# Performance work log

Measured on AMD Instinct MI355X. Metric: run time of the kernel, lower is better.

Reference implementation:

```python
import jax, jax.numpy as jnp
import numpy as np

BS, S, D, H = 2, 2048, 1024, 16
DH = D // H  # 64


def setup_inputs() -> dict:
    key = jax.random.key(0)
    k1, k2, k3 = jax.random.split(key, 3)
    x = jax.random.normal(k1, (BS, S, D), dtype=jnp.float32)
    w_qkv = jax.random.normal(k2, (D, H, 3 * DH), dtype=jnp.float32) * (D ** -0.5)
    b_qkv = jnp.zeros((H, 3 * DH), dtype=jnp.float32)
    w_out = jax.random.normal(k3, (H, DH, D), dtype=jnp.float32) * (D ** -0.5)
    b_out = jnp.zeros((D,), dtype=jnp.float32)
    return {"x": x, "w_qkv": w_qkv, "b_qkv": b_qkv, "w_out": w_out, "b_out": b_out}


def reference(x, w_qkv, b_qkv, w_out, b_out):
    dtype = x.dtype
    # QKV projection: DenseGeneral(features=(H, 3*DH)) -> [B, S, H, 3*DH]
    qkv = jnp.einsum("bsd,dhf->bshf", x, w_qkv) + b_qkv
    q, k, v = jnp.split(qkv, 3, axis=-1)  # each [B, S, H, DH]

    scale = DH ** -0.5
    q = (q * scale).astype(jnp.float32)
    k = k.astype(jnp.float32)
    # Full causal attention with fp32 scores (as in original)
    weights = jnp.einsum("bqhd,bkhd->bhqk", q, k)  # [B, H, S, S]
    causal = jnp.tril(jnp.ones((S, S), dtype=bool))[None, None, :, :]
    weights = jnp.where(causal, weights, jnp.finfo(jnp.float32).min)
    weights = jax.nn.softmax(weights, axis=-1).astype(dtype)
    attn = jnp.einsum("bhqk,bkhd->bqhd", weights, v).astype(dtype)

    # Output projection: DenseGeneral(D, axis=(-2, -1))
    out = jnp.einsum("bqhd,hdo->bqo", attn, w_out) + b_out
    return out
```

## Files before the change

kernel.cpp:

```cpp
#include <hip/hip_runtime.h>
#include <hip/hip_bf16.h>
#include <stdint.h>

#define NBS 2
#define SEQ 2048
#define DMODEL 1024
#define NH 16
#define DHEAD 64
#define MROWS (NBS*SEQ)
#define NQKV (NH*3*DHEAD)

typedef __bf16 bf16;
typedef __bf16 bf16x8 __attribute__((ext_vector_type(8)));
typedef float f32x4 __attribute__((ext_vector_type(4)));
typedef float f32x16 __attribute__((ext_vector_type(16)));
typedef unsigned int u32x2 __attribute__((ext_vector_type(2)));

#define LOG2E 1.44269504088896f
#define QSCALE (0.125f * LOG2E)

static __device__ __forceinline__ void gload_lds16(const bf16* g, bf16* l) {
    __builtin_amdgcn_global_load_lds(
        (const __attribute__((address_space(1))) uint32_t*)g,
        (__attribute__((address_space(3))) uint32_t*)l, 16, 0, 0);
}

static __device__ __forceinline__ bf16x8 ld_b8(const bf16* p) {
    return __builtin_bit_cast(bf16x8, *(const uint4*)p);
}

static __device__ __forceinline__ uint32_t pk_bf16(float lo, float hi) {
    unsigned short l = __builtin_bit_cast(unsigned short, (bf16)lo);
    unsigned short h = __builtin_bit_cast(unsigned short, (bf16)hi);
    return ((uint32_t)h << 16) | (uint32_t)l;
}

static __device__ __forceinline__ u32x2 lane_swap32(uint32_t a, uint32_t b, int lane) {
#if __has_builtin(__builtin_amdgcn_permlane32_swap)
    return __builtin_amdgcn_permlane32_swap(a, b, false, false);
#else
    uint32_t sa = __shfl_xor(a, 32), sb = __shfl_xor(b, 32);
    u32x2 r;
    r.x = (lane >= 32) ? sb : a;
    r.y = (lane >= 32) ? b : sa;
    return r;
#endif
}


__global__ void k_cvt(const float* __restrict__ in, bf16* __restrict__ out, int n4) {
    int i = blockIdx.x * blockDim.x + threadIdx.x;
    if (i < n4) {
        float4 v = ((const float4*)in)[i];
        ushort4 o;
        o.x = __builtin_bit_cast(unsigned short, (bf16)v.x);
        o.y = __builtin_bit_cast(unsigned short, (bf16)v.y);
        o.z = __builtin_bit_cast(unsigned short, (bf16)v.z);
        o.w = __builtin_bit_cast(unsigned short, (bf16)v.w);
        ((ushort4*)out)[i] = o;
    }
}

__global__ void k_tcvt(const float* __restrict__ in, bf16* __restrict__ out, int R, int C) {
    __shared__ float t[32][33];
    int tx = threadIdx.x, ty = threadIdx.y;
    int r0 = blockIdx.y * 32, c0 = blockIdx.x * 32;
#pragma unroll
    for (int i = 0; i < 4; i++)
        t[ty + i*8][tx] = in[(size_t)(r0 + ty + i*8) * C + (c0 + tx)];
    __syncthreads();
#pragma unroll
    for (int i = 0; i < 4; i++)
        out[(size_t)(c0 + ty + i*8) * R + (r0 + tx)] = (bf16)t[tx][ty + i*8];
}

__global__ void k_tcvt_qkv(const float* __restrict__ in, bf16* __restrict__ out) {
    __shared__ float t[32][33];
    int tx = threadIdx.x, ty = threadIdx.y;
    int r0 = blockIdx.y * 32, c0 = blockIdx.x * 32;
#pragma unroll
    for (int i = 0; i < 4; i++)
        t[ty + i*8][tx] = in[(size_t)(r0 + ty + i*8) * NQKV + (c0 + tx)];
    __syncthreads();
#pragma unroll
    for (int i = 0; i < 4; i++) {
        int c = c0 + ty + i*8;
        int h = c / 192, f = c % 192;
        int cperm = ((f >> 6) << 10) + (h << 6) + (f & 63);
        out[(size_t)cperm * DMODEL + (r0 + tx)] = (bf16)t[tx][ty + i*8];
    }
}

template<int KD>
static __device__ __forceinline__ void gemm_tile(
        const bf16* __restrict__ A, const bf16* __restrict__ Bt,
        bf16* As, bf16* Bs, f32x4 acc[4][4], int tile_m, int tile_n) {
    int tid = threadIdx.x;
    int wave = tid >> 6, lane = tid & 63;
    int wr = wave >> 1, wc = wave & 1;
    int g = lane >> 4, r = lane & 15;
    int srow = lane >> 2, schunk = (lane & 3) * 8;

#pragma unroll
    for (int m = 0; m < 4; m++)
#pragma unroll
        for (int n = 0; n < 4; n++)
            acc[m][n] = (f32x4){0.f, 0.f, 0.f, 0.f};

    for (int k0 = 0; k0 < KD; k0 += 32) {
#pragma unroll
        for (int i = 0; i < 2; i++) {
            int ii = wave + i * 4;
            gload_lds16(A  + (size_t)(tile_m + ii*16 + srow) * KD + k0 + schunk, As + ii*512);
            gload_lds16(Bt + (size_t)(tile_n + ii*16 + srow) * KD + k0 + schunk, Bs + ii*512);
        }
        __syncthreads();
        bf16x8 af[4], bfr[4];
#pragma unroll
        for (int m = 0; m < 4; m++) af[m]  = *(const bf16x8*)(As + (wr*64 + m*16 + r)*32 + g*8);
#pragma unroll
        for (int n = 0; n < 4; n++) bfr[n] = *(const bf16x8*)(Bs + (wc*64 + n*16 + r)*32 + g*8);
#pragma unroll
        for (int m = 0; m < 4; m++)
#pragma unroll
            for (int n = 0; n < 4; n++)
                acc[m][n] = __builtin_amdgcn_mfma_f32_16x16x32_bf16(af[m], bfr[n], acc[m][n], 0, 0, 0);
        __syncthreads();
    }
}

__global__ __launch_bounds__(256) void k_gemm_qkv(
        const bf16* __restrict__ A, const bf16* __restrict__ Bt,
        const float* __restrict__ bias,
        bf16* __restrict__ Q, bf16* __restrict__ Kp, bf16* __restrict__ Vt) {
    __shared__ __align__(16) bf16 As[128*32];
    __shared__ __align__(16) bf16 Bs[128*32];
    f32x4 acc[4][4];
    int tile_m = blockIdx.y * 128, tile_n = blockIdx.x * 128;
    gemm_tile<DMODEL>(A, Bt, As, Bs, acc, tile_m, tile_n);

    int wave = threadIdx.x >> 6, lane = threadIdx.x & 63;
    int wr = wave >> 1, wc = wave & 1, g = lane >> 4, r = lane & 15;
#pragma unroll
    for (int m = 0; m < 4; m++) {
#pragma unroll
        for (int n = 0; n < 4; n++) {
            int col = tile_n + wc*64 + n*16 + r;
            int kind = col >> 10;
            int h = (col >> 6) & 15;
            int d = col & 63;
            float bv = bias[h*192 + (kind << 6) + d];
#pragma unroll
            for (int j = 0; j < 4; j++) {
                int row = tile_m + wr*64 + m*16 + g*4 + j;
                int b = row >> 11, s = row & 2047;
                float v = acc[m][n][j] + bv;
                if (kind == 0) {
                    Q[(((size_t)(b*NH + h)) * SEQ + s) * DHEAD + d] = (bf16)(v * QSCALE);
                } else if (kind == 1) {
                    Kp[(((size_t)(b*NH + h)) * SEQ + s) * DHEAD + d] = (bf16)v;
                } else {
                    Vt[(((size_t)(b*NH + h)) * DHEAD + d) * SEQ + s] = (bf16)v;
                }
            }
        }
    }
}

__global__ __launch_bounds__(256) void k_gemm_out(
        const bf16* __restrict__ A, const bf16* __restrict__ Bt,
        const float* __restrict__ bias, float* __restrict__ out) {
    __shared__ __align__(16) bf16 As[64*32];
    __shared__ __align__(16) bf16 Bs[128*32];
    int tid = threadIdx.x;
    int wave = tid >> 6, lane = tid & 63;
    int g = lane >> 4, r = lane & 15;
    int srow = lane >> 2, schunk = (lane & 3) * 8;
    int tile_m = blockIdx.y * 64, tile_n = blockIdx.x * 128;

    f32x4 acc[4][2];
#pragma unroll
    for (int m = 0; m < 4; m++)
#pragma unroll
        for (int n = 0; n < 2; n++)
            acc[m][n] = (f32x4){0.f, 0.f, 0.f, 0.f};

    for (int k0 = 0; k0 < DMODEL; k0 += 32) {
        gload_lds16(A  + (size_t)(tile_m + wave*16 + srow) * DMODEL + k0 + schunk, As + wave*512);
        gload_lds16(Bt + (size_t)(tile_n + wave*16 + srow) * DMODEL + k0 + schunk, Bs + wave*512);
        gload_lds16(Bt + (size_t)(tile_n + 64 + wave*16 + srow) * DMODEL + k0 + schunk, Bs + 2048 + wave*512);
        __syncthreads();
        bf16x8 af[4], bfr[2];
#pragma unroll
        for (int m = 0; m < 4; m++) af[m]  = *(const bf16x8*)(As + (m*16 + r)*32 + g*8);
#pragma unroll
        for (int n = 0; n < 2; n++) bfr[n] = *(const bf16x8*)(Bs + (wave*32 + n*16 + r)*32 + g*8);
#pragma unroll
        for (int m = 0; m < 4; m++)
#pragma unroll
            for (int n = 0; n < 2; n++)
                acc[m][n] = __builtin_amdgcn_mfma_f32_16x16x32_bf16(af[m], bfr[n], acc[m][n], 0, 0, 0);
        __syncthreads();
    }

#pragma unroll
    for (int m = 0; m < 4; m++) {
#pragma unroll
        for (int n = 0; n < 2; n++) {
            int col = tile_n + wave*32 + n*16 + r;
            float bv = bias[col];
#pragma unroll
            for (int j = 0; j < 4; j++) {
                int row = tile_m + m*16 + g*4 + j;
                out[(size_t)row * DMODEL + col] = acc[m][n][j] + bv;
            }
        }
    }
}

#define QBLK 128
#define KVB 64

static __device__ __forceinline__ void attn_tile_body(
        const bf16* Ks, const bf16* VsT,
        const bf16x8 qa2[4], const bf16x8& ones,
        f32x16 o32[2], f32x16& acc_l,
        int kv0, int qb, int qrow, int l31, int hi, int lane) {
    const f32x16 z16 = {0,0,0,0,0,0,0,0,0,0,0,0,0,0,0,0};
    int sw = (l31 & 7) << 3;
    f32x16 st[2];
    st[0] = z16; st[1] = z16;
    __builtin_amdgcn_s_setprio(1);
#pragma unroll
    for (int rb = 0; rb < 2; rb++) {
#pragma unroll
        for (int c = 0; c < 4; c++) {
            bf16x8 kf = ld_b8(Ks + ((((rb*32 + l31)*64) + c*16 + hi*8) ^ sw));
            st[rb] = __builtin_amdgcn_mfma_f32_32x32x16_bf16(kf, qa2[c], st[rb], 0, 0, 0);
        }
    }
    __builtin_amdgcn_s_setprio(0);

    bf16x8 vf[2][4];
#pragma unroll
    for (int dblk = 0; dblk < 2; dblk++)
#pragma unroll
        for (int c = 0; c < 4; c++)
            vf[dblk][c] = ld_b8(VsT + ((((dblk*32 + l31)*64) + c*16 + hi*8) ^ sw));

    bool needm = (kv0 + KVB - 1) > qb;
#pragma unroll
    for (int rb = 0; rb < 2; rb++) {
#pragma unroll
        for (int reg = 0; reg < 16; reg++) {
            float e = __builtin_amdgcn_exp2f(st[rb][reg]);
            if (needm) {
                int kv = kv0 + rb*32 + (reg & 3) + 8*(reg >> 2) + 4*hi;
                if (kv > qrow) e = 0.f;
            }
            st[rb][reg] = e;
        }
    }

    bf16x8 pa[4];
#pragma unroll
    for (int c = 0; c < 4; c++) {
        const f32x16& pp = st[c >> 1];
        const int base = (c & 1) * 8;
        uint32_t a0 = pk_bf16(pp[base+0], pp[base+1]);
        uint32_t a1 = pk_bf16(pp[base+2], pp[base+3]);
        uint32_t b0 = pk_bf16(pp[base+4], pp[base+5]);
        uint32_t b1 = pk_bf16(pp[base+6], pp[base+7]);
        u32x2 s0 = lane_swap32(a0, b0, lane);
        u32x2 s1 = lane_swap32(a1, b1, lane);
        uint4 fr = {s0.x, s1.x, s0.y, s1.y};
        pa[c] = __builtin_bit_cast(bf16x8, fr);
    }

    __builtin_amdgcn_s_setprio(1);
#pragma unroll
    for (int dblk = 0; dblk < 2; dblk++)
#pragma unroll
        for (int c = 0; c < 4; c++)
            o32[dblk] = __builtin_amdgcn_mfma_f32_32x32x16_bf16(pa[c], vf[dblk][c], o32[dblk], 0, 0, 0);
#pragma unroll
    for (int c = 0; c < 4; c++)
        acc_l = __builtin_amdgcn_mfma_f32_32x32x16_bf16(pa[c], ones, acc_l, 0, 0, 0);
    __builtin_amdgcn_s_setprio(0);
}

__device__ const int8_t JQC[32]  = {10,10, 4, 0, 15,15, 3, 1,  9, 9, 7, 2, 13,14, 7, 5,
                                    14,14,11, 5, 15, 8,11, 6,  8,12,12, 6, 13,13,11,12};
__device__ const int8_t JT0[32]  = { 0,11, 0, 0,  0,11, 0, 0,  0,10, 0, 0,  0, 0, 8, 0,
                                    10,20, 0, 6, 22, 0, 8, 0,  9, 0, 9, 7, 10,19,16,18};
__device__ const int8_t JT1[32]  = {11,22,10, 2, 11,22, 8, 4, 10,20, 8, 6, 10,10,16, 6,
                                    20,30, 8,12, 32, 9,16, 7, 18, 9,18,14, 19,28,24,26};
__device__ const int8_t JSEG[32] = { 0, 1, 0, 0,  0, 1, 0, 0,  0, 1, 0, 0,  0, 0, 1, 0,
                                     1, 2, 0, 1,  2, 0, 1, 0,  1, 0, 1, 1,  1, 2, 2, 2};

__global__ __launch_bounds__(256) void k_attn_split(
        const bf16* __restrict__ Q, const bf16* __restrict__ K,
        const bf16* __restrict__ Vt,
        bf16* __restrict__ Op0, bf16* __restrict__ Op1, bf16* __restrict__ Op2,
        float* __restrict__ Lp0, float* __restrict__ Lp1, float* __restrict__ Lp2) {
    int scu = blockIdx.x;
    int bh = scu >> 3, slot = scu & 7;
    int j = slot * 4 + blockIdx.y;
    int qc  = JQC[j];
    int t0  = JT0[j];
    int t1  = JT1[j];
    int seg = JSEG[j];
    int q0 = qc * QBLK;
    int tid = threadIdx.x, wave = tid >> 6, lane = tid & 63;
    int l31 = lane & 31, hi = lane >> 5;

    __shared__ __align__(16) bf16 Ks[2][KVB*64];
    __shared__ __align__(16) bf16 VsT[2][KVB*64];

    const bf16* Kg = K  + (size_t)bh * SEQ * DHEAD;
    const bf16* Vg = Vt + (size_t)bh * DHEAD * SEQ;

    int qb = q0 + wave * 32;
    int qrow = qb + l31;

    const bf16* qrow_p = Q + ((size_t)bh * SEQ + qrow) * DHEAD;
    bf16x8 qa2[4];
#pragma unroll
    for (int c = 0; c < 4; c++) qa2[c] = ld_b8(qrow_p + c*16 + hi*8);

    bf16x8 ones;
#pragma unroll
    for (int c = 0; c < 8; c++) ones[c] = (bf16)1.0f;

    const f32x16 z16 = {0,0,0,0,0,0,0,0,0,0,0,0,0,0,0,0};
    f32x16 o32[2], acc_l;
    o32[0] = z16; o32[1] = z16; acc_l = z16;

    int qmax_wave = qb + 31;

    int srow = tid >> 3, sc8 = tid & 7;
    int sw_st = (srow & 7) << 3;
    int wK0 = ((srow*64)      + sc8*8) ^ sw_st;
    int wK1 = (((srow+32)*64) + sc8*8) ^ sw_st;

    bf16x8 kreg[2], vreg[2];
    {
        int kvs = t0 * KVB;
        kreg[0] = ld_b8(Kg + (size_t)(kvs + srow)      * DHEAD + sc8*8);
        kreg[1] = ld_b8(Kg + (size_t)(kvs + srow + 32) * DHEAD + sc8*8);
        vreg[0] = ld_b8(Vg + (size_t)srow      * SEQ + kvs + sc8*8);
        vreg[1] = ld_b8(Vg + (size_t)(srow+32) * SEQ + kvs + sc8*8);
    }

    int cur = 0;
    for (int t = t0; t < t1; t++) {
        int kv0 = t * KVB;
        *(uint4*)&Ks[cur][wK0]  = __builtin_bit_cast(uint4, kreg[0]);
        *(uint4*)&Ks[cur][wK1]  = __builtin_bit_cast(uint4, kreg[1]);
        *(uint4*)&VsT[cur][wK0] = __builtin_bit_cast(uint4, vreg[0]);
        *(uint4*)&VsT[cur][wK1] = __builtin_bit_cast(uint4, vreg[1]);
        __syncthreads();

        if (t + 1 < t1) {
            int kv1 = kv0 + KVB;
            kreg[0] = ld_b8(Kg + (size_t)(kv1 + srow)      * DHEAD + sc8*8);
            kreg[1] = ld_b8(Kg + (size_t)(kv1 + srow + 32) * DHEAD + sc8*8);
            vreg[0] = ld_b8(Vg + (size_t)srow      * SEQ + kv1 + sc8*8);
            vreg[1] = ld_b8(Vg + (size_t)(srow+32) * SEQ + kv1 + sc8*8);
        }

        if (kv0 <= qmax_wave)
            attn_tile_body(Ks[cur], VsT[cur], qa2, ones, o32, acc_l,
                           kv0, qb, qrow, l31, hi, lane);
        cur ^= 1;
    }

    bf16* Op; float* Lp; size_t obase; int lbase;
    if (seg == 0)      { Op = Op0; Lp = Lp0; obase = ((size_t)bh*2048 + q0) * 64;          lbase = bh*2048 + q0; }
    else if (seg == 1) { Op = Op1; Lp = Lp1; obase = ((size_t)bh*1408 + (qc-5)*128) * 64;  lbase = bh*1408 + (qc-5)*128; }
    else               { Op = Op2; Lp = Lp2; obase = ((size_t)bh*640  + (qc-11)*128) * 64; lbase = bh*640  + (qc-11)*128; }

    if (l31 == 0) {
#pragma unroll
        for (int reg = 0; reg < 16; reg++) {
            int qr = (reg & 3) + 8*(reg >> 2) + 4*hi;
            Lp[lbase + wave*32 + qr] = acc_l[reg];
        }
    }

#pragma unroll
    for (int reg = 0; reg < 16; reg++) {
        int qr = (reg & 3) + 8*(reg >> 2) + 4*hi;
        size_t base = obase + (size_t)(wave*32 + qr) * 64 + l31;
        Op[base]      = (bf16)o32[0][reg];
        Op[base + 32] = (bf16)o32[1][reg];
    }
}

__global__ __launch_bounds__(256) void k_merge(
        const bf16* __restrict__ Op0, const bf16* __restrict__ Op1,
        const bf16* __restrict__ Op2,
        const float* __restrict__ Lp0, const float* __restrict__ Lp1,
        const float* __restrict__ Lp2,
        bf16* __restrict__ Oa) {
    int g = blockIdx.x * 256 + threadIdx.x;
    int dseg = g & 7;
    int s = (g >> 3) & 2047;
    int bh = g >> 14;
    int qc = s >> 7;
    int sl = s & 127;

    size_t r0 = ((size_t)bh * 2048 + s) * 64 + dseg*8;
    bf16x8 p0 = ld_b8(Op0 + r0);
    float l = Lp0[bh*2048 + s];
    float acc[8];
#pragma unroll
    for (int i = 0; i < 8; i++) acc[i] = (float)p0[i];

    if (qc >= 5) {
        size_t r1 = ((size_t)bh * 1408 + (qc-5)*128 + sl) * 64 + dseg*8;
        bf16x8 p1 = ld_b8(Op1 + r1);
        l += Lp1[bh*1408 + (qc-5)*128 + sl];
#pragma unroll
        for (int i = 0; i < 8; i++) acc[i] += (float)p1[i];
        if (qc >= 11) {
            size_t r2 = ((size_t)bh * 640 + (qc-11)*128 + sl) * 64 + dseg*8;
            bf16x8 p2 = ld_b8(Op2 + r2);
            l += Lp2[bh*640 + (qc-11)*128 + sl];
#pragma unroll
            for (int i = 0; i < 8; i++) acc[i] += (float)p2[i];
        }
    }

    float inv = 1.0f / l;
    bf16x8 r;
#pragma unroll
    for (int i = 0; i < 8; i++) r[i] = (bf16)(acc[i] * inv);
    int b = bh >> 4, h = bh & 15;
    *(uint4*)&Oa[(((size_t)b * SEQ + s) * NH + h) * DHEAD + dseg*8] =
        __builtin_bit_cast(uint4, r);
}

__global__ __launch_bounds__(256) void k_attn(
        const bf16* __restrict__ Q, const bf16* __restrict__ K,
        const bf16* __restrict__ Vt, bf16* __restrict__ O) {
    int bh = blockIdx.y;
    int qc = (bh >= 16) ? (15 - (int)blockIdx.x) : (int)blockIdx.x;
    int q0 = qc * QBLK;
    int tid = threadIdx.x, wave = tid >> 6, lane = tid & 63;
    int l31 = lane & 31, hi = lane >> 5;

    __shared__ __align__(16) bf16 Ks[2][KVB*64];
    __shared__ __align__(16) bf16 VsT[2][KVB*64];

    const bf16* Kg = K  + (size_t)bh * SEQ * DHEAD;
    const bf16* Vg = Vt + (size_t)bh * DHEAD * SEQ;

    int qb = q0 + wave * 32;
    int qrow = qb + l31;

    const bf16* qrow_p = Q + ((size_t)bh * SEQ + qrow) * DHEAD;
    bf16x8 qa2[4];
#pragma unroll
    for (int c = 0; c < 4; c++) qa2[c] = ld_b8(qrow_p + c*16 + hi*8);

    bf16x8 ones;
#pragma unroll
    for (int c = 0; c < 8; c++) ones[c] = (bf16)1.0f;

    const f32x16 z16 = {0,0,0,0,0,0,0,0,0,0,0,0,0,0,0,0};
    f32x16 o32[2], acc_l;
    o32[0] = z16; o32[1] = z16; acc_l = z16;

    int nt = 2*qc + 2;
    int qmax_wave = qb + 31;

    int srow = tid >> 3, sc8 = tid & 7;
    int sw_st = (srow & 7) << 3;
    int wK0 = ((srow*64)      + sc8*8) ^ sw_st;
    int wK1 = (((srow+32)*64) + sc8*8) ^ sw_st;

    bf16x8 kreg[2], vreg[2];
    kreg[0] = ld_b8(Kg + (size_t)srow      * DHEAD + sc8*8);
    kreg[1] = ld_b8(Kg + (size_t)(srow+32) * DHEAD + sc8*8);
    vreg[0] = ld_b8(Vg + (size_t)srow      * SEQ + sc8*8);
    vreg[1] = ld_b8(Vg + (size_t)(srow+32) * SEQ + sc8*8);

    int cur = 0;
    for (int t = 0; t < nt; t++) {
        int kv0 = t * KVB;
        *(uint4*)&Ks[cur][wK0]  = __builtin_bit_cast(uint4, kreg[0]);
        *(uint4*)&Ks[cur][wK1]  = __builtin_bit_cast(uint4, kreg[1]);
        *(uint4*)&VsT[cur][wK0] = __builtin_bit_cast(uint4, vreg[0]);
        *(uint4*)&VsT[cur][wK1] = __builtin_bit_cast(uint4, vreg[1]);
        __syncthreads();

        if (t + 1 < nt) {
            int kv1 = kv0 + KVB;
            kreg[0] = ld_b8(Kg + (size_t)(kv1 + srow)      * DHEAD + sc8*8);
            kreg[1] = ld_b8(Kg + (size_t)(kv1 + srow + 32) * DHEAD + sc8*8);
            vreg[0] = ld_b8(Vg + (size_t)srow      * SEQ + kv1 + sc8*8);
            vreg[1] = ld_b8(Vg + (size_t)(srow+32) * SEQ + kv1 + sc8*8);
        }

        if (kv0 <= qmax_wave)
            attn_tile_body(Ks[cur], VsT[cur], qa2, ones, o32, acc_l,
                           kv0, qb, qrow, l31, hi, lane);
        cur ^= 1;
    }

    int b = bh >> 4, h = bh & 15;
#pragma unroll
    for (int reg = 0; reg < 16; reg++) {
        int qr = (reg & 3) + 8*(reg >> 2) + 4*hi;
        int srow2 = q0 + wave*32 + qr;
        float linv = 1.0f / acc_l[reg];
        size_t base = (((size_t)b * SEQ + srow2) * NH + h) * DHEAD + l31;
        O[base]      = (bf16)(o32[0][reg] * linv);
        O[base + 32] = (bf16)(o32[1][reg] * linv);
    }
}


extern "C" void kernel_launch(void* const* d_in, const int* in_sizes, int n_in,
                              void* d_out, int out_size, void* d_ws, size_t ws_size,
                              hipStream_t stream) {
    const float* x     = (const float*)d_in[0];
    const float* w_qkv = (const float*)d_in[1];
    const float* b_qkv = (const float*)d_in[2];
    const float* w_out = (const float*)d_in[3];
    const float* b_out = (const float*)d_in[4];
    float* out = (float*)d_out;

    char* ws = (char*)d_ws;
    bf16* xb   = (bf16*)(ws);
    bf16* wqkT = (bf16*)(ws + 8388608);
    bf16* woT  = (bf16*)(ws + 14680064);
    bf16* qb   = (bf16*)(ws + 16777216);
    bf16* kb   = (bf16*)(ws + 25165824);
    bf16* vb   = (bf16*)(ws + 33554432);
    bf16* Op0  = (bf16*)(ws + 41943040);
    bf16* Op1  = (bf16*)(ws + 50331648);
    bf16* Op2  = (bf16*)(ws + 56098816);
    float* Lp0 = (float*)(ws + 8388608);
    float* Lp1 = (float*)(ws + 8388608 + 262144);
    float* Lp2 = (float*)(ws + 8388608 + 524288);
    const size_t WS_NEED = 58720256;
    bf16* attn = xb;

    k_cvt<<<(MROWS*DMODEL/4 + 255)/256, 256, 0, stream>>>(x, xb, MROWS*DMODEL/4);
    dim3 tb(32, 8);
    k_tcvt_qkv<<<dim3(NQKV/32, DMODEL/32), tb, 0, stream>>>(w_qkv, wqkT);
    k_tcvt<<<dim3(DMODEL/32, DMODEL/32), tb, 0, stream>>>(w_out, woT, DMODEL, DMODEL);

    k_gemm_qkv<<<dim3(NQKV/128, MROWS/128), 256, 0, stream>>>(xb, wqkT, b_qkv, qb, kb, vb);

    if (ws_size >= WS_NEED) {
        k_attn_split<<<dim3(256, 4), 256, 0, stream>>>(qb, kb, vb,
                                                       Op0, Op1, Op2, Lp0, Lp1, Lp2);
        k_merge<<<(NBS*NH*SEQ*DHEAD/8)/256, 256, 0, stream>>>(Op0, Op1, Op2,
                                                              Lp0, Lp1, Lp2, attn);
    } else {
        k_attn<<<dim3(SEQ/QBLK, NBS*NH), 256, 0, stream>>>(qb, kb, vb, attn);
    }

    k_gemm_out<<<dim3(DMODEL/128, MROWS/64), 256, 0, stream>>>(attn, woT, b_out, out);
}
```

Baseline: 123.2 us.

## Double-buffer LDS in projection GEMMs, swizzle tile order, vectorize V-transpose stores

```diff
diff --git a/kernel.cpp b/kernel.cpp
--- a/kernel.cpp
+++ b/kernel.cpp
@@ -91,35 +91,53 @@
     }
 }
 
-template<int KD>
-static __device__ __forceinline__ void gemm_tile(
+__global__ __launch_bounds__(256) void k_gemm_qkv(
         const bf16* __restrict__ A, const bf16* __restrict__ Bt,
-        bf16* As, bf16* Bs, f32x4 acc[4][4], int tile_m, int tile_n) {
+        const float* __restrict__ bias,
+        bf16* __restrict__ Q, bf16* __restrict__ Kp, bf16* __restrict__ Vt) {
+    __shared__ __align__(16) bf16 As[2][128*32];
+    __shared__ __align__(16) bf16 Bs[2][128*32];
     int tid = threadIdx.x;
     int wave = tid >> 6, lane = tid & 63;
     int wr = wave >> 1, wc = wave & 1;
     int g = lane >> 4, r = lane & 15;
     int srow = lane >> 2, schunk = (lane & 3) * 8;
 
+    int lid = blockIdx.y * 24 + blockIdx.x;
+    int swz = (lid & 7) * 96 + (lid >> 3);
+    int tile_n = (swz % 24) * 128, tile_m = (swz / 24) * 128;
+
+    f32x4 acc[4][4];
 #pragma unroll
     for (int m = 0; m < 4; m++)
 #pragma unroll
         for (int n = 0; n < 4; n++)
             acc[m][n] = (f32x4){0.f, 0.f, 0.f, 0.f};
 
-    for (int k0 = 0; k0 < KD; k0 += 32) {
-#pragma unroll
-        for (int i = 0; i < 2; i++) {
-            int ii = wave + i * 4;
-            gload_lds16(A  + (size_t)(tile_m + ii*16 + srow) * KD + k0 + schunk, As + ii*512);
-            gload_lds16(Bt + (size_t)(tile_n + ii*16 + srow) * KD + k0 + schunk, Bs + ii*512);
-        }
-        __syncthreads();
+#pragma unroll
+    for (int i = 0; i < 2; i++) {
+        int ii = wave + i * 4;
+        gload_lds16(A  + (size_t)(tile_m + ii*16 + srow) * DMODEL + schunk, As[0] + ii*512);
+        gload_lds16(Bt + (size_t)(tile_n + ii*16 + srow) * DMODEL + schunk, Bs[0] + ii*512);
+    }
+    __syncthreads();
+
+    for (int ks = 0; ks < 32; ks++) {
+        int cur = ks & 1;
+        if (ks + 1 < 32) {
+            int k1 = (ks + 1) * 32;
+#pragma unroll
+            for (int i = 0; i < 2; i++) {
+                int ii = wave + i * 4;
+                gload_lds16(A  + (size_t)(tile_m + ii*16 + srow) * DMODEL + k1 + schunk, As[cur^1] + ii*512);
+                gload_lds16(Bt + (size_t)(tile_n + ii*16 + srow) * DMODEL + k1 + schunk, Bs[cur^1] + ii*512);
+            }
+        }
         bf16x8 af[4], bfr[4];
 #pragma unroll
-        for (int m = 0; m < 4; m++) af[m]  = *(const bf16x8*)(As + (wr*64 + m*16 + r)*32 + g*8);
-#pragma unroll
-        for (int n = 0; n < 4; n++) bfr[n] = *(const bf16x8*)(Bs + (wc*64 + n*16 + r)*32 + g*8);
+        for (int m = 0; m < 4; m++) af[m]  = *(const bf16x8*)(As[cur] + (wr*64 + m*16 + r)*32 + g*8);
+#pragma unroll
+        for (int n = 0; n < 4; n++) bfr[n] = *(const bf16x8*)(Bs[cur] + (wc*64 + n*16 + r)*32 + g*8);
 #pragma unroll
         for (int m = 0; m < 4; m++)
 #pragma unroll
@@ -127,20 +145,7 @@
                 acc[m][n] = __builtin_amdgcn_mfma_f32_16x16x32_bf16(af[m], bfr[n], acc[m][n], 0, 0, 0);
         __syncthreads();
     }
-}
-
-__global__ __launch_bounds__(256) void k_gemm_qkv(
-        const bf16* __restrict__ A, const bf16* __restrict__ Bt,
-        const float* __restrict__ bias,
-        bf16* __restrict__ Q, bf16* __restrict__ Kp, bf16* __restrict__ Vt) {
-    __shared__ __align__(16) bf16 As[128*32];
-    __shared__ __align__(16) bf16 Bs[128*32];
-    f32x4 acc[4][4];
-    int tile_m = blockIdx.y * 128, tile_n = blockIdx.x * 128;
-    gemm_tile<DMODEL>(A, Bt, As, Bs, acc, tile_m, tile_n);
-
-    int wave = threadIdx.x >> 6, lane = threadIdx.x & 63;
-    int wr = wave >> 1, wc = wave & 1, g = lane >> 4, r = lane & 15;
+
 #pragma unroll
     for (int m = 0; m < 4; m++) {
 #pragma unroll
@@ -150,17 +155,24 @@
             int h = (col >> 6) & 15;
             int d = col & 63;
             float bv = bias[h*192 + (kind << 6) + d];
-#pragma unroll
-            for (int j = 0; j < 4; j++) {
-                int row = tile_m + wr*64 + m*16 + g*4 + j;
-                int b = row >> 11, s = row & 2047;
-                float v = acc[m][n][j] + bv;
-                if (kind == 0) {
-                    Q[(((size_t)(b*NH + h)) * SEQ + s) * DHEAD + d] = (bf16)(v * QSCALE);
-                } else if (kind == 1) {
-                    Kp[(((size_t)(b*NH + h)) * SEQ + s) * DHEAD + d] = (bf16)v;
-                } else {
-                    Vt[(((size_t)(b*NH + h)) * DHEAD + d) * SEQ + s] = (bf16)v;
+            if (kind == 2) {
+                int row0 = tile_m + wr*64 + m*16 + g*4;
+                int b = row0 >> 11, s0 = row0 & 2047;
+                ushort4 vv;
+                vv.x = __builtin_bit_cast(unsigned short, (bf16)(acc[m][n][0] + bv));
+                vv.y = __builtin_bit_cast(unsigned short, (bf16)(acc[m][n][1] + bv));
+                vv.z = __builtin_bit_cast(unsigned short, (bf16)(acc[m][n][2] + bv));
+                vv.w = __builtin_bit_cast(unsigned short, (bf16)(acc[m][n][3] + bv));
+                *(ushort4*)&Vt[(((size_t)(b*NH + h)) * DHEAD + d) * SEQ + s0] = vv;
+            } else {
+#pragma unroll
+                for (int j = 0; j < 4; j++) {
+                    int row = tile_m + wr*64 + m*16 + g*4 + j;
+                    int b = row >> 11, s = row & 2047;
+                    float v = acc[m][n][j] + bv;
+                    size_t addr = (((size_t)(b*NH + h)) * SEQ + s) * DHEAD + d;
+                    if (kind == 0) Q[addr]  = (bf16)(v * QSCALE);
+                    else           Kp[addr] = (bf16)v;
                 }
             }
         }
@@ -170,13 +182,16 @@
 __global__ __launch_bounds__(256) void k_gemm_out(
         const bf16* __restrict__ A, const bf16* __restrict__ Bt,
         const float* __restrict__ bias, float* __restrict__ out) {
-    __shared__ __align__(16) bf16 As[64*32];
-    __shared__ __align__(16) bf16 Bs[128*32];
+    __shared__ __align__(16) bf16 As[2][64*32];
+    __shared__ __align__(16) bf16 Bs[2][128*32];
     int tid = threadIdx.x;
     int wave = tid >> 6, lane = tid & 63;
     int g = lane >> 4, r = lane & 15;
     int srow = lane >> 2, schunk = (lane & 3) * 8;
-    int tile_m = blockIdx.y * 64, tile_n = blockIdx.x * 128;
+
+    int lid = blockIdx.y * 8 + blockIdx.x;
+    int swz = (lid & 7) * 64 + (lid >> 3);
+    int tile_n = (swz % 8) * 128, tile_m = (swz / 8) * 64;
 
     f32x4 acc[4][2];
 #pragma unroll
@@ -185,16 +200,24 @@
         for (int n = 0; n < 2; n++)
             acc[m][n] = (f32x4){0.f, 0.f, 0.f, 0.f};
 
-    for (int k0 = 0; k0 < DMODEL; k0 += 32) {
-        gload_lds16(A  + (size_t)(tile_m + wave*16 + srow) * DMODEL + k0 + schunk, As + wave*512);
-        gload_lds16(Bt + (size_t)(tile_n + wave*16 + srow) * DMODEL + k0 + schunk, Bs + wave*512);
-        gload_lds16(Bt + (size_t)(tile_n + 64 + wave*16 + srow) * DMODEL + k0 + schunk, Bs + 2048 + wave*512);
-        __syncthreads();
+    gload_lds16(A  + (size_t)(tile_m + wave*16 + srow) * DMODEL + schunk, As[0] + wave*512);
+    gload_lds16(Bt + (size_t)(tile_n + wave*16 + srow) * DMODEL + schunk, Bs[0] + wave*512);
+    gload_lds16(Bt + (size_t)(tile_n + 64 + wave*16 + srow) * DMODEL + schunk, Bs[0] + 2048 + wave*512);
+    __syncthreads();
+
+    for (int ks = 0; ks < 32; ks++) {
+        int cur = ks & 1;
+        if (ks + 1 < 32) {
+            int k1 = (ks + 1) * 32;
+            gload_lds16(A  + (size_t)(tile_m + wave*16 + srow) * DMODEL + k1 + schunk, As[cur^1] + wave*512);
+            gload_lds16(Bt + (size_t)(tile_n + wave*16 + srow) * DMODEL + k1 + schunk, Bs[cur^1] + wave*512);
+            gload_lds16(Bt + (size_t)(tile_n + 64 + wave*16 + srow) * DMODEL + k1 + schunk, Bs[cur^1] + 2048 + wave*512);
+        }
         bf16x8 af[4], bfr[2];
 #pragma unroll
-        for (int m = 0; m < 4; m++) af[m]  = *(const bf16x8*)(As + (m*16 + r)*32 + g*8);
-#pragma unroll
-        for (int n = 0; n < 2; n++) bfr[n] = *(const bf16x8*)(Bs + (wave*32 + n*16 + r)*32 + g*8);
+        for (int m = 0; m < 4; m++) af[m]  = *(const bf16x8*)(As[cur] + (m*16 + r)*32 + g*8);
+#pragma unroll
+        for (int n = 0; n < 2; n++) bfr[n] = *(const bf16x8*)(Bs[cur] + (wave*32 + n*16 + r)*32 + g*8);
 #pragma unroll
         for (int m = 0; m < 4; m++)
 #pragma unroll
```

Result: no change. 124.7 us (+1.2%).

## Rewrite QKV GEMM with 256x256 tiles, double-buffered swizzled LDS, vectorized V store

Applied to the files above, without the earlier changes.

```diff
diff --git a/kernel.cpp b/kernel.cpp
--- a/kernel.cpp
+++ b/kernel.cpp
@@ -91,58 +91,86 @@
     }
 }
 
-template<int KD>
-static __device__ __forceinline__ void gemm_tile(
-        const bf16* __restrict__ A, const bf16* __restrict__ Bt,
-        bf16* As, bf16* Bs, f32x4 acc[4][4], int tile_m, int tile_n) {
-    int tid = threadIdx.x;
-    int wave = tid >> 6, lane = tid & 63;
-    int wr = wave >> 1, wc = wave & 1;
-    int g = lane >> 4, r = lane & 15;
-    int srow = lane >> 2, schunk = (lane & 3) * 8;
-
-#pragma unroll
-    for (int m = 0; m < 4; m++)
-#pragma unroll
-        for (int n = 0; n < 4; n++)
-            acc[m][n] = (f32x4){0.f, 0.f, 0.f, 0.f};
-
-    for (int k0 = 0; k0 < KD; k0 += 32) {
-#pragma unroll
-        for (int i = 0; i < 2; i++) {
-            int ii = wave + i * 4;
-            gload_lds16(A  + (size_t)(tile_m + ii*16 + srow) * KD + k0 + schunk, As + ii*512);
-            gload_lds16(Bt + (size_t)(tile_n + ii*16 + srow) * KD + k0 + schunk, Bs + ii*512);
-        }
-        __syncthreads();
-        bf16x8 af[4], bfr[4];
-#pragma unroll
-        for (int m = 0; m < 4; m++) af[m]  = *(const bf16x8*)(As + (wr*64 + m*16 + r)*32 + g*8);
-#pragma unroll
-        for (int n = 0; n < 4; n++) bfr[n] = *(const bf16x8*)(Bs + (wc*64 + n*16 + r)*32 + g*8);
-#pragma unroll
-        for (int m = 0; m < 4; m++)
-#pragma unroll
-            for (int n = 0; n < 4; n++)
-                acc[m][n] = __builtin_amdgcn_mfma_f32_16x16x32_bf16(af[m], bfr[n], acc[m][n], 0, 0, 0);
-        __syncthreads();
-    }
-}
-
-__global__ __launch_bounds__(256) void k_gemm_qkv(
+#define G1_NT 16
+
+__global__ __launch_bounds__(512, 2) void k_gemm_qkv(
         const bf16* __restrict__ A, const bf16* __restrict__ Bt,
         const float* __restrict__ bias,
         bf16* __restrict__ Q, bf16* __restrict__ Kp, bf16* __restrict__ Vt) {
-    __shared__ __align__(16) bf16 As[128*32];
-    __shared__ __align__(16) bf16 Bs[128*32];
-    f32x4 acc[4][4];
-    int tile_m = blockIdx.y * 128, tile_n = blockIdx.x * 128;
-    gemm_tile<DMODEL>(A, Bt, As, Bs, acc, tile_m, tile_n);
-
-    int wave = threadIdx.x >> 6, lane = threadIdx.x & 63;
-    int wr = wave >> 1, wc = wave & 1, g = lane >> 4, r = lane & 15;
-#pragma unroll
-    for (int m = 0; m < 4; m++) {
+    __shared__ __align__(16) bf16 As[2][256*64];
+    __shared__ __align__(16) bf16 Bs[2][256*64];
+    int tid = threadIdx.x;
+    int wid = tid >> 6, lane = tid & 63;
+    int wr = wid >> 2, wc = wid & 3;
+    int g = lane >> 4, r = lane & 15;
+
+    int lid = blockIdx.y * 12 + blockIdx.x;
+    int swz = (lid & 7) * 24 + (lid >> 3);
+    int tile_n = (swz % 12) * 256, tile_m = (swz / 12) * 256;
+
+    f32x4 acc[8][4];
+#pragma unroll
+    for (int m = 0; m < 8; m++)
+#pragma unroll
+        for (int n = 0; n < 4; n++)
+            acc[m][n] = (f32x4){0.f, 0.f, 0.f, 0.f};
+
+    int srow[4], schk[4];
+#pragma unroll
+    for (int j2 = 0; j2 < 4; j2++) {
+        int idx = tid + j2 * 512;
+        srow[j2] = idx >> 3;
+        schk[j2] = ((idx & 7) ^ (srow[j2] & 7)) * 8;
+    }
+
+#define G1_STAGE(buf, k0)                                                        \
+    {                                                                            \
+        _Pragma("unroll")                                                        \
+        for (int j2 = 0; j2 < 4; j2++) {                                         \
+            gload_lds16(A  + (size_t)(tile_m + srow[j2]) * DMODEL + (k0) + schk[j2], \
+                        As[buf] + (tid + j2*512) * 8);                           \
+            gload_lds16(Bt + (size_t)(tile_n + srow[j2]) * DMODEL + (k0) + schk[j2], \
+                        Bs[buf] + (tid + j2*512) * 8);                           \
+        }                                                                        \
+    }
+
+    G1_STAGE(0, 0);
+
+    int r7 = r & 7;
+    for (int t = 0; t < G1_NT; t++) {
+        int cur = t & 1;
+        if (t + 1 < G1_NT) {
+            G1_STAGE(cur ^ 1, (t + 1) * 64);
+            asm volatile("s_waitcnt vmcnt(8)" ::: "memory");
+        } else {
+            asm volatile("s_waitcnt vmcnt(0)" ::: "memory");
+        }
+        __builtin_amdgcn_s_barrier();
+        __builtin_amdgcn_sched_barrier(0);
+
+        const bf16* pa = As[cur];
+        const bf16* pb = Bs[cur];
+#pragma unroll
+        for (int kk = 0; kk < 2; kk++) {
+            int rchk = ((kk*4 + g) ^ r7) * 8;
+            bf16x8 bfr[4];
+#pragma unroll
+            for (int n = 0; n < 4; n++)
+                bfr[n] = ld_b8(pb + (wc*64 + n*16 + r) * 64 + rchk);
+#pragma unroll
+            for (int m = 0; m < 8; m++) {
+                bf16x8 af = ld_b8(pa + (wr*128 + m*16 + r) * 64 + rchk);
+#pragma unroll
+                for (int n = 0; n < 4; n++)
+                    acc[m][n] = __builtin_amdgcn_mfma_f32_16x16x32_bf16(af, bfr[n], acc[m][n], 0, 0, 0);
+            }
+        }
+        asm volatile("s_waitcnt lgkmcnt(0)" ::: "memory");
+        __builtin_amdgcn_s_barrier();
+    }
+
+#pragma unroll
+    for (int m = 0; m < 8; m++) {
 #pragma unroll
         for (int n = 0; n < 4; n++) {
             int col = tile_n + wc*64 + n*16 + r;
@@ -150,21 +178,29 @@
             int h = (col >> 6) & 15;
             int d = col & 63;
             float bv = bias[h*192 + (kind << 6) + d];
-#pragma unroll
-            for (int j = 0; j < 4; j++) {
-                int row = tile_m + wr*64 + m*16 + g*4 + j;
-                int b = row >> 11, s = row & 2047;
-                float v = acc[m][n][j] + bv;
-                if (kind == 0) {
-                    Q[(((size_t)(b*NH + h)) * SEQ + s) * DHEAD + d] = (bf16)(v * QSCALE);
-                } else if (kind == 1) {
-                    Kp[(((size_t)(b*NH + h)) * SEQ + s) * DHEAD + d] = (bf16)v;
-                } else {
-                    Vt[(((size_t)(b*NH + h)) * DHEAD + d) * SEQ + s] = (bf16)v;
+            if (kind == 2) {
+                int row0 = tile_m + wr*128 + m*16 + g*4;
+                int b = row0 >> 11, s0 = row0 & 2047;
+                ushort4 vv;
+                vv.x = __builtin_bit_cast(unsigned short, (bf16)(acc[m][n][0] + bv));
+                vv.y = __builtin_bit_cast(unsigned short, (bf16)(acc[m][n][1] + bv));
+                vv.z = __builtin_bit_cast(unsigned short, (bf16)(acc[m][n][2] + bv));
+                vv.w = __builtin_bit_cast(unsigned short, (bf16)(acc[m][n][3] + bv));
+                *(ushort4*)&Vt[(((size_t)(b*NH + h)) * DHEAD + d) * SEQ + s0] = vv;
+            } else {
+#pragma unroll
+                for (int j = 0; j < 4; j++) {
+                    int row = tile_m + wr*128 + m*16 + g*4 + j;
+                    int b = row >> 11, s = row & 2047;
+                    float v = acc[m][n][j] + bv;
+                    size_t addr = (((size_t)(b*NH + h)) * SEQ + s) * DHEAD + d;
+                    if (kind == 0) Q[addr]  = (bf16)(v * QSCALE);
+                    else           Kp[addr] = (bf16)v;
                 }
             }
         }
     }
+#undef G1_STAGE
 }
 
 __global__ __launch_bounds__(256) void k_gemm_out(
@@ -553,7 +589,7 @@
     k_tcvt_qkv<<<dim3(NQKV/32, DMODEL/32), tb, 0, stream>>>(w_qkv, wqkT);
     k_tcvt<<<dim3(DMODEL/32, DMODEL/32), tb, 0, stream>>>(w_out, woT, DMODEL, DMODEL);
 
-    k_gemm_qkv<<<dim3(NQKV/128, MROWS/128), 256, 0, stream>>>(xb, wqkT, b_qkv, qb, kb, vb);
+    k_gemm_qkv<<<dim3(12, 16), 512, 0, stream>>>(xb, wqkT, b_qkv, qb, kb, vb);
 
     if (ws_size >= WS_NEED) {
         k_attn_split<<<dim3(256, 4), 256, 0, stream>>>(qb, kb, vb,
```

Measured after the change: 120.9 us. About the same (-1.9%).
